# Kernel optimization log

Hardware: AMD Instinct MI355X
Metric: run time of the kernel (lower is better)

Reference implementation:

```python
import jax, jax.numpy as jnp
import numpy as np

NT, NS, NH, NG = 365, 1024, 64, 32
NW = NH * 8 + 2


def setup_inputs() -> dict:
    key = jax.random.key(0)
    k1, k2, k3, k4 = jax.random.split(key, 4)
    std = 1.0 / np.sqrt(NH)
    x = jax.random.normal(k1, (NT, NS, 4), dtype=jnp.float32)
    # make P (precip) nonnegative and T1 < T2 plausible-ish; math is still generic
    xc = jax.random.normal(k2, (NS, NG), dtype=jnp.float32)
    fc_w = jax.random.uniform(k3, (NW, NG), minval=-std, maxval=std, dtype=jnp.float32)
    fc_b = jax.random.uniform(k4, (NW,), minval=-std, maxval=std, dtype=jnp.float32)
    return {"x": x, "xc": xc, "fc_w": fc_w, "fc_b": fc_b}


def reference(x, xc, fc_w, fc_b):
    nh = NH
    P, E, T1, T2 = x[..., 0], x[..., 1], x[..., 2], x[..., 3]  # each [nt, ns]
    Ta = (T1 + T2) * 0.5
    # rain/snow partition: rP = 1 - arccos((T1+T2)/(T2-T1))/3.1415, masked
    valid = (T1 < 0) & (T2 > 0)
    denom = jnp.where(valid, T2 - T1, 1.0)
    ratio = jnp.clip(jnp.where(valid, (T1 + T2) / denom, 0.0), -0.999999, 0.999999)
    rP = 1.0 - jnp.arccos(ratio) / 3.1415
    rP = jnp.where(T1 >= 0, 1.0, rP)
    rP = jnp.where(T2 <= 0, 0.0, rP)
    Ps = (1.0 - rP) * P  # snow   [nt, ns]
    Pl = rP * P          # liquid [nt, ns]

    w = xc @ fc_w.T + fc_b  # [ns, nh*8+2]
    gm = jnp.exp(w[:, :nh]) + 1.0
    ge = jax.nn.sigmoid(w[:, nh:2 * nh]) * 2.0
    go = jax.nn.sigmoid(w[:, 2 * nh:3 * nh])
    gl = jnp.exp(w[:, 3 * nh:4 * nh] * 2.0)
    ga = jax.nn.softmax(w[:, 4 * nh:5 * nh], axis=1)  # Dropout in eval mode = identity
    gb = jax.nn.sigmoid(w[:, 5 * nh:6 * nh])
    qb = jax.nn.relu(w[:, -1]) / nh  # [ns]
    kb = jax.nn.sigmoid(w[:, 6 * nh:7 * nh]) / 10.0
    gi = jax.nn.sigmoid(w[:, 7 * nh:8 * nh])

    ns = P.shape[1]
    init = (jnp.zeros((ns, nh), jnp.float32),) * 3  # S0, H0, G0

    def step(carry, inp):
        S0, H0, G0 = carry
        Ps_k, Pl_k, Ta_k, E_k = inp  # each [ns]
        S = S0 + Ps_k[:, None]
        Sm = jnp.minimum(S0, jax.nn.relu(Ta_k[:, None] * gm))  # snowmelt
        H = jax.nn.relu(H0 + Sm + Pl_k[:, None] * gi - E_k[:, None] * ge)
        Q1 = jax.nn.relu(H - gl)
        Q2a = jnp.minimum(H, gl) * go
        Q2 = Q2a * (1.0 - gb)
        G = G0 + Q2a * gb
        Q3 = G * kb
        H0n = jnp.minimum(H - Q2a, gl)
        G0n = G - Q3
        S0n = S - Sm
        Y = jnp.sum((Q1 + Q2 + Q3 + qb[:, None]) * ga, axis=1)  # [ns]
        return (S0n, H0n, G0n), Y

    _, Yout = jax.lax.scan(step, init, (Ps, Pl, Ta, E))
    return Yout  # [nt, ns]
```

## Files before the change

kernel.cpp:

```cpp
#include <hip/hip_runtime.h>
#include <math.h>

#define NT_ 365
#define NS_ 1024
#define NH_ 64
#define NG_ 32
#define NW_ 514
#define CH_ 64
#define NCHUNK_ 6
#define YPAD_ 65

__device__ __forceinline__ float sigmoidf(float v) {
  return 1.0f / (1.0f + expf(-v));
}

__device__ __forceinline__ float blane(float v, int j) {
  return __int_as_float(__builtin_amdgcn_readlane(__float_as_int(v), j));
}

struct Met { float Ps, Pl, Tr, E; };

__device__ __forceinline__ Met compute_met(float4 xv) {
  const float P = xv.x, E = xv.y, T1 = xv.z, T2 = xv.w;
  const float Ta = (T1 + T2) * 0.5f;
  float rP;
  if (T2 <= 0.0f) {
    rP = 0.0f;
  } else if (T1 >= 0.0f) {
    rP = 1.0f;
  } else {
    float r = (T1 + T2) / (T2 - T1);
    r = fminf(fmaxf(r, -0.999999f), 0.999999f);
    rP = 1.0f - acosf(r) * (1.0f / 3.1415f);
  }
  Met m;
  m.Ps = (1.0f - rP) * P;
  m.Pl = rP * P;
  m.Tr = fmaxf(Ta, 0.0f);
  m.E  = E;
  return m;
}

__global__ __launch_bounds__(256) void waternet_scan(
    const float* __restrict__ x,
    const float* __restrict__ xc,
    const float* __restrict__ fc_w,
    const float* __restrict__ fc_b,
    float* __restrict__ out)
{
  __shared__ float ytile[4][CH_ * YPAD_];

  const int tid  = threadIdx.x;
  const int lane = tid & 63;
  const int wv   = tid >> 6;
  const int site = (blockIdx.x << 2) + wv;
  const int us   = __builtin_amdgcn_readfirstlane(site);
  const float4* xp = (const float4*)x;

  float4 xcur = xp[lane * NS_ + site];

  float acc[8];
#pragma unroll
  for (int k = 0; k < 8; ++k) acc[k] = fc_b[k * NH_ + lane];
  float accq = fc_b[NW_ - 1];

  const float4* xcq = (const float4*)(xc + us * NG_);
  const float4* wq4 = (const float4*)fc_w;
#pragma unroll
  for (int g4 = 0; g4 < NG_ / 4; ++g4) {
    const float4 xv = xcq[g4];
#pragma unroll
    for (int k = 0; k < 8; ++k) {
      const float4 w = wq4[(k * NH_ + lane) * (NG_ / 4) + g4];
      acc[k] = fmaf(xv.x, w.x, acc[k]);
      acc[k] = fmaf(xv.y, w.y, acc[k]);
      acc[k] = fmaf(xv.z, w.z, acc[k]);
      acc[k] = fmaf(xv.w, w.w, acc[k]);
    }
    {
      const float4 w = wq4[(NW_ - 1) * (NG_ / 4) + g4];
      accq = fmaf(xv.x, w.x, accq);
      accq = fmaf(xv.y, w.y, accq);
      accq = fmaf(xv.z, w.z, accq);
      accq = fmaf(xv.w, w.w, accq);
    }
  }

  const float gm = expf(acc[0]) + 1.0f;
  const float ge = sigmoidf(acc[1]) * 2.0f;
  const float go = sigmoidf(acc[2]);
  const float gl = expf(acc[3] * 2.0f);
  float mx = acc[4];
#pragma unroll
  for (int mm = 32; mm >= 1; mm >>= 1) mx = fmaxf(mx, __shfl_xor(mx, mm, 64));
  const float ex = expf(acc[4] - mx);
  float sm = ex;
#pragma unroll
  for (int mm = 32; mm >= 1; mm >>= 1) sm += __shfl_xor(sm, mm, 64);
  const float ga = ex / sm;
  const float gb = sigmoidf(acc[5]);
  const float kb = sigmoidf(acc[6]) * 0.1f;
  const float gi = sigmoidf(acc[7]);
  const float qb = fmaxf(accq, 0.0f) * (1.0f / NH_);
  const float kb1m    = 1.0f - kb;
  const float gb1m_ga = (1.0f - gb) * ga;
  const float nge     = -ge;

  float S0 = 0.0f, H0 = 0.0f, G0 = 0.0f;
  Met m = compute_met(xcur);

  float*       yw = &ytile[wv][lane];
  const float* yr = &ytile[wv][lane * YPAD_];
  float* outp = out + lane * NS_ + site;

  for (int c = 0; c < NCHUNK_; ++c) {
    float4 xnext;
    const bool more = (c + 1 < NCHUNK_);
    if (more) {
      const int t = (c + 1) * CH_ + lane;
      xnext = (t < NT_) ? xp[t * NS_ + site]
                        : make_float4(0.0f, 0.0f, 0.0f, 0.0f);
    }

#pragma unroll
    for (int j = 0; j < CH_; ++j) {
      const float Ps = blane(m.Ps, j);
      const float Pl = blane(m.Pl, j);
      const float Tr = blane(m.Tr, j);
      const float E  = blane(m.E,  j);

      const float S     = S0 + Ps;
      const float Sm    = fminf(S0, Tr * gm);
      const float addin = fmaf(E, nge, Pl * gi);
      const float H     = fmaxf(H0 + Sm + addin, 0.0f);
      const float M     = fminf(H, gl);
      const float Q1    = H - M;
      const float Q2a   = M * go;
      const float G     = fmaf(Q2a, gb, G0);
      const float Q3    = G * kb;
      H0 = fminf(H - Q2a, gl);
      G0 = G * kb1m;
      S0 = S - Sm;
      yw[j * YPAD_] = fmaf(Q1 + Q3, ga, Q2a * gb1m_ga);
    }

    float t0 = 0.0f, t1 = 0.0f, t2 = 0.0f, t3 = 0.0f;
#pragma unroll
    for (int h = 0; h < CH_; h += 4) {
      t0 += yr[h + 0];
      t1 += yr[h + 1];
      t2 += yr[h + 2];
      t3 += yr[h + 3];
    }
    const float tot = (t0 + t1) + (t2 + t3);
    const int t_out = c * CH_ + lane;
    if (t_out < NT_) *outp = tot + qb;
    outp += CH_ * NS_;

    if (more) m = compute_met(xnext);
  }
}

extern "C" void kernel_launch(void* const* d_in, const int* in_sizes, int n_in,
                              void* d_out, int out_size, void* d_ws, size_t ws_size,
                              hipStream_t stream) {
  const float* x    = (const float*)d_in[0];
  const float* xc   = (const float*)d_in[1];
  const float* fc_w = (const float*)d_in[2];
  const float* fc_b = (const float*)d_in[3];
  float* out = (float*)d_out;

  hipLaunchKernelGGL(waternet_scan, dim3(NS_ / 4), dim3(256), 0, stream,
                     x, xc, fc_w, fc_b, out);
}
```

Baseline: 90.66 us.

## Stage forcing via LDS broadcast, double-buffer Y tile, fold step algebra

Per-step forcing values are now staged in shared memory as float4 and read back as a uniform LDS load, replacing four readlane broadcasts per step. The Y tile is double-buffered so the reduction of the previous chunk's hidden-unit sums is interleaved with the current chunk's recurrence, overlapping LDS reads with the serial dependency chain. The per-step arithmetic is also rewritten to shorten the dependency chain: snowmelt is expressed through max(S0-melt,0), and the output terms are folded into fewer FMAs. The cost is more LDS use and extra LDS traffic, plus possible reassociation differences in floating-point results.

```diff
diff --git a/kernel.cpp b/kernel.cpp
--- a/kernel.cpp
+++ b/kernel.cpp
@@ -14,13 +14,7 @@
   return 1.0f / (1.0f + expf(-v));
 }
 
-__device__ __forceinline__ float blane(float v, int j) {
-  return __int_as_float(__builtin_amdgcn_readlane(__float_as_int(v), j));
-}
-
-struct Met { float Ps, Pl, Tr, E; };
-
-__device__ __forceinline__ Met compute_met(float4 xv) {
+__device__ __forceinline__ float4 compute_met(float4 xv) {
   const float P = xv.x, E = xv.y, T1 = xv.z, T2 = xv.w;
   const float Ta = (T1 + T2) * 0.5f;
   float rP;
@@ -33,11 +27,11 @@
     r = fminf(fmaxf(r, -0.999999f), 0.999999f);
     rP = 1.0f - acosf(r) * (1.0f / 3.1415f);
   }
-  Met m;
-  m.Ps = (1.0f - rP) * P;
-  m.Pl = rP * P;
-  m.Tr = fmaxf(Ta, 0.0f);
-  m.E  = E;
+  float4 m;
+  m.x = (1.0f - rP) * P;
+  m.y = rP * P;
+  m.z = fmaxf(Ta, 0.0f);
+  m.w = E;
   return m;
 }
 
@@ -48,7 +42,8 @@
     const float* __restrict__ fc_b,
     float* __restrict__ out)
 {
-  __shared__ float ytile[4][CH_ * YPAD_];
+  __shared__ float  ytile[4][2][CH_ * YPAD_];
+  __shared__ float4 smet[4][CH_];
 
   const int tid  = threadIdx.x;
   const int lane = tid & 63;
@@ -102,62 +97,74 @@
   const float kb = sigmoidf(acc[6]) * 0.1f;
   const float gi = sigmoidf(acc[7]);
   const float qb = fmaxf(accq, 0.0f) * (1.0f / NH_);
-  const float kb1m    = 1.0f - kb;
-  const float gb1m_ga = (1.0f - gb) * ga;
-  const float nge     = -ge;
+  const float kb1m = 1.0f - kb;
+  const float nge  = -ge;
+  const float gq1  = go * (1.0f - gb) - 1.0f;
 
   float S0 = 0.0f, H0 = 0.0f, G0 = 0.0f;
-  Met m = compute_met(xcur);
+  const int vofs = lane * NS_ + site;
 
-  float*       yw = &ytile[wv][lane];
-  const float* yr = &ytile[wv][lane * YPAD_];
-  float* outp = out + lane * NS_ + site;
+  smet[wv][lane] = compute_met(xcur);
 
-  for (int c = 0; c < NCHUNK_; ++c) {
-    float4 xnext;
-    const bool more = (c + 1 < NCHUNK_);
-    if (more) {
-      const int t = (c + 1) * CH_ + lane;
-      xnext = (t < NT_) ? xp[t * NS_ + site]
-                        : make_float4(0.0f, 0.0f, 0.0f, 0.0f);
-    }
+  auto step = [&](const float4 mt, float* ywaddr) {
+    const float melt = mt.z * gm;
+    const float dmx  = fmaxf(S0 - melt, 0.0f);
+    const float hs   = H0 + S0;
+    S0 = dmx + mt.x;
+    const float t3 = fmaf(mt.y, gi, hs - dmx);
+    const float H  = fmaxf(fmaf(mt.w, nge, t3), 0.0f);
+    const float M  = fminf(H, gl);
+    const float Q2a = M * go;
+    H0 = fminf(H - Q2a, gl);
+    const float G = fmaf(Q2a, gb, G0);
+    G0 = G * kb1m;
+    *ywaddr = fmaf(G, kb, fmaf(M, gq1, H)) * ga;
+  };
 
+  {
+    float4 xnext = xp[(CH_ + lane) * NS_ + site];
+    float* yw = &ytile[wv][0][lane];
+    const float4* mp = &smet[wv][0];
+#pragma unroll
+    for (int j = 0; j < CH_; ++j) step(mp[j], yw + j * YPAD_);
+    smet[wv][lane] = compute_met(xnext);
+  }
+
+  for (int c = 1; c < NCHUNK_; ++c) {
+    int tn = (c + 1) * CH_ + lane;
+    tn = (tn < NT_) ? tn : (NT_ - 1);
+    const float4 xnext = xp[tn * NS_ + site];
+
+    float*       yw = &ytile[wv][c & 1][lane];
+    const float* yr = &ytile[wv][(c - 1) & 1][lane * YPAD_];
+    const float4* mp = &smet[wv][0];
+    float r0 = 0.0f, r1 = 0.0f, r2 = 0.0f, r3 = 0.0f;
 #pragma unroll
     for (int j = 0; j < CH_; ++j) {
-      const float Ps = blane(m.Ps, j);
-      const float Pl = blane(m.Pl, j);
-      const float Tr = blane(m.Tr, j);
-      const float E  = blane(m.E,  j);
+      if ((j & 3) == 0) {
+        r0 += yr[j + 0];
+        r1 += yr[j + 1];
+        r2 += yr[j + 2];
+        r3 += yr[j + 3];
+      }
+      step(mp[j], yw + j * YPAD_);
+    }
+    out[vofs + (c - 1) * CH_ * NS_] = ((r0 + r1) + (r2 + r3)) + qb;
+    smet[wv][lane] = compute_met(xnext);
+  }
 
-      const float S     = S0 + Ps;
-      const float Sm    = fminf(S0, Tr * gm);
-      const float addin = fmaf(E, nge, Pl * gi);
-      const float H     = fmaxf(H0 + Sm + addin, 0.0f);
-      const float M     = fminf(H, gl);
-      const float Q1    = H - M;
-      const float Q2a   = M * go;
-      const float G     = fmaf(Q2a, gb, G0);
-      const float Q3    = G * kb;
-      H0 = fminf(H - Q2a, gl);
-      G0 = G * kb1m;
-      S0 = S - Sm;
-      yw[j * YPAD_] = fmaf(Q1 + Q3, ga, Q2a * gb1m_ga);
-    }
-
-    float t0 = 0.0f, t1 = 0.0f, t2 = 0.0f, t3 = 0.0f;
+  {
+    const float* yr = &ytile[wv][1][lane * YPAD_];
+    float r0 = 0.0f, r1 = 0.0f, r2 = 0.0f, r3 = 0.0f;
 #pragma unroll
     for (int h = 0; h < CH_; h += 4) {
-      t0 += yr[h + 0];
-      t1 += yr[h + 1];
-      t2 += yr[h + 2];
-      t3 += yr[h + 3];
+      r0 += yr[h + 0];
+      r1 += yr[h + 1];
+      r2 += yr[h + 2];
+      r3 += yr[h + 3];
     }
-    const float tot = (t0 + t1) + (t2 + t3);
-    const int t_out = c * CH_ + lane;
-    if (t_out < NT_) *outp = tot + qb;
-    outp += CH_ * NS_;
-
-    if (more) m = compute_met(xnext);
+    if (lane < NT_ - 5 * CH_)
+      out[vofs + 5 * CH_ * NS_] = ((r0 + r1) + (r2 + r3)) + qb;
   }
 }
 
```

Result: no change. 90.21 us (-0.5%).
